# Optimization experiments

Hardware: AMD Instinct MI355X
Metric: run time of the kernel (lower is better)

Reference implementation:

```python
import jax, jax.numpy as jnp
import numpy as np

N_USER = 150_000
M_ITEM = 30_000
N_NODES = N_USER + M_ITEM
D = 64                      # embedding_dim
N_LAYERS = 3                # gcn_layer_number
E = 600_000                 # user-item interactions (symmetric nnz = 2E)
B = 1024
NUM_RATE, NUM_GENRE, NUM_DIR, NUM_ACT = 6, 25, 2186, 8030
NUM_GENDER, NUM_AGE, NUM_OCC, NUM_ZIP = 2, 7, 21, 3402
H1, H2 = 64, 64             # first/second fc hidden dims
FC1_IN = D * 10


def setup_inputs() -> dict:
    key = jax.random.key(0)
    ks = jax.random.split(key, 24)
    # aux features: 0/1 values are valid indices for every categorical field
    aux_info = jax.random.randint(ks[0], (B, 10246), 0, 2, dtype=jnp.int32)
    user_ids = jax.random.randint(ks[1], (B,), 0, N_USER, dtype=jnp.int32)
    item_ids = jax.random.randint(ks[2], (B,), 0, M_ITEM, dtype=jnp.int32)
    # bipartite graph: random interactions, symmetric normalized adjacency
    u = jax.random.randint(ks[3], (E,), 0, N_USER, dtype=jnp.int32)
    i = jax.random.randint(ks[4], (E,), 0, M_ITEM, dtype=jnp.int32) + N_USER
    graph_row = jnp.concatenate([u, i])
    graph_col = jnpph = jnp.concatenate([i, u]) if False else jnp.concatenate([i, u])
    deg = jax.ops.segment_sum(jnp.ones((2 * E,), jnp.float32), graph_row, num_segments=N_NODES)
    dinv = jnp.where(deg > 0, jax.lax.rsqrt(jnp.maximum(deg, 1.0)), 0.0)
    graph_val = dinv[graph_row] * dinv[graph_col]
    s = 0.1
    nrm = lambda k, shp: (jax.random.normal(k, shp, jnp.float32) * s)
    return {
        "aux_info": aux_info, "user_ids": user_ids, "item_ids": item_ids,
        "graph_row": graph_row, "graph_col": graph_col, "graph_val": graph_val,
        "rate_tab": nrm(ks[5], (NUM_RATE, D)),
        "genre_W": nrm(ks[6], (NUM_GENRE, D)),
        "director_W": nrm(ks[7], (NUM_DIR, D)),
        "actor_W": nrm(ks[8], (NUM_ACT, D)),
        "gender_tab": nrm(ks[9], (NUM_GENDER, D)),
        "age_tab": nrm(ks[10], (NUM_AGE, D)),
        "occ_tab": nrm(ks[11], (NUM_OCC, D)),
        "area_tab": nrm(ks[12], (NUM_ZIP, D)),
        "user_rel": nrm(ks[13], (N_USER, D)),
        "item_rel": nrm(ks[14], (M_ITEM, D)),
        "fc1_W": nrm(ks[15], (FC1_IN, H1)), "fc1_b": jnp.zeros((H1,), jnp.float32),
        "fc2_W": nrm(ks[16], (H1, H2)), "fc2_b": jnp.zeros((H2,), jnp.float32),
        "out_W": nrm(ks[17], (H2, 1)), "out_b": jnp.zeros((1,), jnp.float32),
    }


def _lightgcn(user_rel, item_rel, row, col, val):
    # LightGCN: repeated SpMM D^-1/2 A D^-1/2 @ emb, mean over layer outputs
    emb = jnp.concatenate([user_rel, item_rel], axis=0)      # [N, D]
    acc = emb
    for _ in range(N_LAYERS):
        emb = jax.ops.segment_sum(val[:, None] * emb[col], row, num_segments=N_NODES)
        acc = acc + emb
    light = acc / (N_LAYERS + 1)
    return light[:N_USER], light[N_USER:]


def _multi_hot(idx_int, W):
    x = idx_int.astype(jnp.float32)
    return (x @ W) / jnp.sum(x, axis=1, keepdims=True)


def reference(aux_info, user_ids, item_ids, graph_row, graph_col, graph_val,
              rate_tab, genre_W, director_W, actor_W,
              gender_tab, age_tab, occ_tab, area_tab,
              user_rel, item_rel,
              fc1_W, fc1_b, fc2_W, fc2_b, out_W, out_b):
    rate_idx = aux_info[:, 0]
    genre_idx = aux_info[:, 1:26]
    director_idx = aux_info[:, 26:2212]
    actor_idx = aux_info[:, 2212:10242]
    gender_idx = aux_info[:, 10242]
    age_idx = aux_info[:, 10243]
    occ_idx = aux_info[:, 10244]
    area_idx = aux_info[:, 10245]

    item_emb = jnp.concatenate([
        rate_tab[rate_idx],
        _multi_hot(genre_idx, genre_W),
        _multi_hot(director_idx, director_W),
        _multi_hot(actor_idx, actor_W),
    ], axis=1)                                               # [B, 4D]
    user_emb = jnp.concatenate([
        gender_tab[gender_idx], age_tab[age_idx],
        occ_tab[occ_idx], area_tab[area_idx],
    ], axis=1)                                               # [B, 4D]

    all_users, all_items = _lightgcn(user_rel, item_rel, graph_row, graph_col, graph_val)
    X = jnp.concatenate([item_emb, user_emb,
                         all_users[user_ids], all_items[item_ids]], axis=1)  # [B, 10D]
    X = jax.nn.relu(X @ fc1_W + fc1_b)
    X = jax.nn.relu(X @ fc2_W + fc2_b)
    return X @ out_W + out_b                                 # [B, 1]
```

## Files before the change

kernel.cpp:

```cpp
#include <hip/hip_runtime.h>
#include <hip/hip_bf16.h>
#include <hip/hip_fp16.h>

#define N_USER 150000
#define M_ITEM 30000
#define N_NODES 180000
#define E2 1200000
#define BATCH 1024
#define AUX_W 10246
#define KP_G 32
#define KP_D 2208
#define KP_A 8064
#define NBKT 265
#define WT_BLKS 2576
#define BCNT_BLKS 293
#define MH_BLKS 672

typedef __attribute__((ext_vector_type(8))) short short8;
typedef __attribute__((ext_vector_type(8))) unsigned short ushort8_t;
typedef __attribute__((ext_vector_type(4))) float f32x4;

__device__ __forceinline__ int bucket_of(int r) {
    return r < N_USER ? (r >> 10) : 147 + ((r - N_USER) >> 8);
}

__device__ __forceinline__ int detect_f32(const void* probe) {
    float v = __bfloat162float(((const __hip_bfloat16*)probe)[threadIdx.x & 63]);
    unsigned long long m = __ballot(!(fabsf(v) < 1000.0f));
    return __popcll(m) > 8;
}

struct CvtSeg { const void* src; float* dst; int n; int blk0; };
struct CvtBatch { CvtSeg seg[16]; };

__global__ void __launch_bounds__(256) k_prep(CvtBatch cb, int cvtBlks,
                                              const void* Wg, const void* Wd, const void* Wa,
                                              unsigned short* WtG, unsigned short* WtD, unsigned short* WtA,
                                              const int* __restrict__ grow, int* __restrict__ bucket_tot,
                                              const void* probe) {
    int blk = blockIdx.x, tid = threadIdx.x;
    if (blk < cvtBlks) {
        int isf32 = detect_f32(probe);
        int si = 0;
        #pragma unroll
        for (int i = 0; i < 16; ++i) if (blk >= cb.seg[i].blk0) si = i;
        const CvtSeg sg = cb.seg[si];
        int i = (blk - sg.blk0) * 256 + tid;
        if (i >= sg.n) return;
        if (isf32) sg.dst[i] = ((const float*)sg.src)[i];
        else       sg.dst[i] = __bfloat162float(((const __hip_bfloat16*)sg.src)[i]);
        return;
    }
    if (blk < cvtBlks + WT_BLKS) {
        int isf32 = detect_f32(probe);
        int t = (blk - cvtBlks) * 256 + tid;
        if (t >= (KP_G + KP_D + KP_A) * 64) return;
        int kp = t >> 6, n = t & 63;
        int k, K; const void* src; unsigned short* dst;
        if (kp < KP_G)              { k = kp;               K = 25;   src = Wg; dst = WtG; }
        else if (kp < KP_G + KP_D)  { k = kp - KP_G;        K = 2186; src = Wd; dst = WtD; }
        else                        { k = kp - KP_G - KP_D; K = 8030; src = Wa; dst = WtA; }
        unsigned short v = 0;
        if (k < K) {
            if (isf32) {
                __hip_bfloat16 h = __float2bfloat16(((const float*)src)[(size_t)k * 64 + n]);
                v = *(unsigned short*)&h;
            } else {
                v = ((const unsigned short*)src)[(size_t)k * 64 + n];
            }
        }
        dst[(((size_t)(k >> 5) * 64 + n) * 4 + ((k >> 3) & 3)) * 8 + (k & 7)] = v;
        return;
    }
    __shared__ int h[NBKT];
    for (int i = tid; i < NBKT; i += 256) h[i] = 0;
    __syncthreads();
    int idx0 = (blk - cvtBlks - WT_BLKS) * 4096;
    #pragma unroll
    for (int k = 0; k < 16; ++k) {
        int i = idx0 + k * 256 + tid;
        if (i < E2) atomicAdd(&h[bucket_of(grow[i])], 1);
    }
    __syncthreads();
    for (int i = tid; i < NBKT; i += 256) if (h[i]) atomicAdd(&bucket_tot[i], h[i]);
}

__global__ void __launch_bounds__(512) k_bscan(const int* __restrict__ bucket_tot,
                                               int* __restrict__ bucket_base,
                                               int* __restrict__ bucketcur) {
    __shared__ int s[512];
    int tid = threadIdx.x;
    s[tid] = (tid < NBKT) ? bucket_tot[tid] : 0;
    __syncthreads();
    for (int off = 1; off < 512; off <<= 1) {
        int v = (tid >= off) ? s[tid - off] : 0;
        __syncthreads();
        s[tid] += v;
        __syncthreads();
    }
    int excl = tid ? s[tid - 1] : 0;
    bucket_base[tid] = excl;
    if (tid < NBKT) bucketcur[tid] = excl;
}

__device__ void mhgemm_body(int blk, const int* __restrict__ aux,
                            const unsigned short* __restrict__ WtG,
                            const unsigned short* __restrict__ WtD,
                            const unsigned short* __restrict__ WtA,
                            float* __restrict__ Xmh, float* __restrict__ cntf) {
    int seg, rb, k0, klen, Kseg, auxoff;
    const unsigned short* Wt;
    if (blk < 16)       { seg = 0; rb = blk;                      k0 = 0;              klen = 25;                  Kseg = 25;   auxoff = 1;    Wt = WtG; }
    else if (blk < 160) { int t = blk - 16;  seg = 1; rb = t & 15; k0 = (t >> 4) * 256; klen = min(256, 2186 - k0); Kseg = 2186; auxoff = 26;   Wt = WtD; }
    else                { int t = blk - 160; seg = 2; rb = t & 15; k0 = (t >> 4) * 256; klen = min(256, 8030 - k0); Kseg = 8030; auxoff = 2212; Wt = WtA; }
    int lane = threadIdx.x & 63, wave = threadIdx.x >> 6;
    int m = lane & 15, quad = lane >> 4;
    int row = rb * 64 + wave * 16 + m;
    const int* arow = aux + (size_t)row * AUX_W + auxoff;

    f32x4 acc0 = {0.f,0.f,0.f,0.f}, acc1 = acc0, acc2 = acc0, acc3 = acc0;
    int isum = 0;
    int nchunk = (klen + 31) >> 5;
    int pa[8], na[8];
    auto lda = [&](int kci, int (&A)[8]) {
        int kb = k0 + kci * 32 + quad * 8;
        if (kb + 8 <= Kseg) {
            #pragma unroll
            for (int j = 0; j < 8; ++j) A[j] = arow[kb + j];
        } else {
            #pragma unroll
            for (int j = 0; j < 8; ++j) A[j] = (kb + j < Kseg) ? arow[kb + j] : 0;
        }
    };
    lda(0, pa);
    for (int kci = 0; kci < nchunk; ++kci) {
        if (kci + 1 < nchunk) lda(kci + 1, na);
        union { unsigned u[4]; short8 s; } af;
        af.u[0] = (unsigned)pa[0] * 16256u + (unsigned)pa[1] * 0x3F800000u;
        af.u[1] = (unsigned)pa[2] * 16256u + (unsigned)pa[3] * 0x3F800000u;
        af.u[2] = (unsigned)pa[4] * 16256u + (unsigned)pa[5] * 0x3F800000u;
        af.u[3] = (unsigned)pa[6] * 16256u + (unsigned)pa[7] * 0x3F800000u;
        isum += pa[0] + pa[1] + pa[2] + pa[3] + pa[4] + pa[5] + pa[6] + pa[7];
        size_t kcg = (size_t)(k0 >> 5) + kci;
        const unsigned short* bp = Wt + ((kcg * 64 + m) * 4 + quad) * 8;
        short8 b0 = *(const short8*)(bp);
        short8 b1 = *(const short8*)(bp + 512);
        short8 b2 = *(const short8*)(bp + 1024);
        short8 b3 = *(const short8*)(bp + 1536);
        acc0 = __builtin_amdgcn_mfma_f32_16x16x32_bf16(af.s, b0, acc0, 0, 0, 0);
        acc1 = __builtin_amdgcn_mfma_f32_16x16x32_bf16(af.s, b1, acc1, 0, 0, 0);
        acc2 = __builtin_amdgcn_mfma_f32_16x16x32_bf16(af.s, b2, acc2, 0, 0, 0);
        acc3 = __builtin_amdgcn_mfma_f32_16x16x32_bf16(af.s, b3, acc3, 0, 0, 0);
        #pragma unroll
        for (int j = 0; j < 8; ++j) pa[j] = na[j];
    }
    float asum = (float)isum;
    asum += __shfl_xor(asum, 16);
    asum += __shfl_xor(asum, 32);
    if (quad == 0) atomicAdd(&cntf[seg * BATCH + row], asum);
    float* xbase = Xmh + ((size_t)seg * BATCH + rb * 64 + wave * 16 + quad * 4) * 64;
    #pragma unroll
    for (int reg = 0; reg < 4; ++reg) {
        float* xr = xbase + (size_t)reg * 64;
        atomicAdd(&xr[ 0 + m], acc0[reg]);
        atomicAdd(&xr[16 + m], acc1[reg]);
        atomicAdd(&xr[32 + m], acc2[reg]);
        atomicAdd(&xr[48 + m], acc3[reg]);
    }
}

__global__ void __launch_bounds__(256) k_p1(const int* __restrict__ grow, const int* __restrict__ gcol,
                                            int* __restrict__ bucketcur, int2* __restrict__ binned,
                                            const int* __restrict__ aux,
                                            const unsigned short* __restrict__ WtG,
                                            const unsigned short* __restrict__ WtD,
                                            const unsigned short* __restrict__ WtA,
                                            float* __restrict__ Xmh, float* __restrict__ cntf) {
    if (blockIdx.x < MH_BLKS) {
        mhgemm_body(blockIdx.x, aux, WtG, WtD, WtA, Xmh, cntf);
        return;
    }
    __shared__ int h1[NBKT], base1[NBKT];
    int tid = threadIdx.x;
    for (int i = tid; i < NBKT; i += 256) h1[i] = 0;
    __syncthreads();
    int idx0 = (blockIdx.x - MH_BLKS) * 4096;
    int r[16], c[16];
    #pragma unroll
    for (int k = 0; k < 16; ++k) {
        int i = idx0 + k * 256 + tid;
        if (i < E2) {
            r[k] = grow[i]; c[k] = gcol[i];
            atomicAdd(&h1[bucket_of(r[k])], 1);
        } else r[k] = -1;
    }
    __syncthreads();
    for (int i = tid; i < NBKT; i += 256) {
        base1[i] = h1[i] ? atomicAdd(&bucketcur[i], h1[i]) : 0;
        h1[i] = 0;
    }
    __syncthreads();
    #pragma unroll
    for (int k = 0; k < 16; ++k) {
        if (r[k] >= 0) {
            int b = bucket_of(r[k]);
            int p = base1[b] + atomicAdd(&h1[b], 1);
            binned[p] = make_int2(r[k], c[k]);
        }
    }
}

__global__ void __launch_bounds__(256) k_p2(const int2* __restrict__ binned, const int* __restrict__ bb,
                                            int* __restrict__ cols, int2* __restrict__ moffs,
                                            float* __restrict__ dinv, float* __restrict__ dsq,
                                            float* __restrict__ gsc) {
    __shared__ int h[1024];
    __shared__ int ws2[256];
    int b = blockIdx.x, tid = threadIdx.x;
    int r0, r1;
    if (b < 147) { r0 = b << 10; r1 = min((b + 1) << 10, N_USER); }
    else         { r0 = N_USER + ((b - 147) << 8); r1 = min(N_USER + ((b - 146) << 8), N_NODES); }
    int s0 = bb[b], e0 = bb[b + 1];
    for (int i = tid; i < 1024; i += 256) h[i] = 0;
    __syncthreads();
    for (int j = s0 + tid; j < e0; j += 256) atomicAdd(&h[binned[j].x - r0], 1);
    __syncthreads();
    int t0 = tid * 4;
    int a0 = h[t0], a1 = h[t0 + 1], a2 = h[t0 + 2], a3 = h[t0 + 3];
    ws2[tid] = a0 + a1 + a2 + a3;
    __syncthreads();
    for (int off = 1; off < 256; off <<= 1) {
        int v = (tid >= off) ? ws2[tid - off] : 0;
        __syncthreads();
        ws2[tid] += v;
        __syncthreads();
    }
    int excl = tid ? ws2[tid - 1] : 0;
    int ex[4] = { excl, excl + a0, excl + a0 + a1, excl + a0 + a1 + a2 };
    int ac[4] = { a0, a1, a2, a3 };
    #pragma unroll
    for (int i = 0; i < 4; ++i) {
        int row = r0 + t0 + i;
        if (row < r1) {
            moffs[row] = make_int2(s0 + ex[i], s0 + ex[i] + ac[i]);
            float deg = (float)ac[i];
            bool nz = deg > 0.f;
            dinv[row] = nz ? rsqrtf(deg) : 0.f;
            dsq[row]  = nz ? 1.f / deg  : 0.f;
            gsc[row]  = nz ? sqrtf(deg) : 0.f;
        }
        h[t0 + i] = ex[i];
    }
    __syncthreads();
    for (int j = s0 + tid; j < e0; j += 256) {
        int2 e = binned[j];
        int p = s0 + atomicAdd(&h[e.x - r0], 1);
        cols[p] = e.y << 7;
    }
}

__global__ void __launch_bounds__(256) k_cvt_fused(const void* rawU, const void* rawI,
                                                   const float* __restrict__ dinv,
                                                   __half* __restrict__ emb,
                                                   float* __restrict__ tacc,
                                                   const int* __restrict__ uids,
                                                   const int* __restrict__ iids, int cvtN,
                                                   const int2* __restrict__ moffs,
                                                   const int* __restrict__ cols,
                                                   int2* __restrict__ moffs2) {
    int blk = blockIdx.x;
    if (blk < cvtN) {
        int isf32 = detect_f32(rawU);
        int q = blk * 256 + threadIdx.x;
        if (q >= N_NODES * 8) return;
        int r = q >> 3;
        const void* src; size_t qq;
        if (r < N_USER) { src = rawU; qq = (size_t)q; }
        else            { src = rawI; qq = (size_t)q - (size_t)N_USER * 8; }
        float d = dinv[r];
        float f[8];
        if (isf32) {
            float4 a = ((const float4*)src)[qq * 2], b = ((const float4*)src)[qq * 2 + 1];
            f[0]=a.x; f[1]=a.y; f[2]=a.z; f[3]=a.w; f[4]=b.x; f[5]=b.y; f[6]=b.z; f[7]=b.w;
        } else {
            ushort8_t u = ((const ushort8_t*)src)[qq];
            #pragma unroll
            for (int i = 0; i < 8; ++i) {
                unsigned short us = u[i];
                f[i] = __bfloat162float(*(__hip_bfloat16*)&us);
            }
        }
        ushort8_t o;
        #pragma unroll
        for (int i = 0; i < 8; ++i) {
            __half h = __float2half(f[i] * d);
            o[i] = *(unsigned short*)&h;
        }
        ((ushort8_t*)emb)[(size_t)q] = o;
        return;
    }
    if (blk < cvtN + 512) {
        int lane = threadIdx.x & 63;
        int t = (blk - cvtN) * 4 + (threadIdx.x >> 6);
        int r = (t < BATCH) ? uids[t] : (N_USER + iids[t - BATCH]);
        int2 se = moffs[r];
        if (lane == 0) moffs2[r] = se;
        for (int j = se.x + lane; j < se.y; j += 64) {
            int c = (unsigned)cols[j] >> 7;
            moffs2[c] = moffs[c];
        }
        return;
    }
    {
        int isf32 = detect_f32(rawU);
        int lane = threadIdx.x & 63;
        int t = (blk - cvtN - 512) * 4 + (threadIdx.x >> 6);
        const void* src; size_t ri;
        if (t < BATCH) { src = rawU; ri = (size_t)uids[t]; }
        else           { src = rawI; ri = (size_t)iids[t - BATCH]; }
        float v;
        if (isf32) v = ((const float*)src)[ri * 64 + lane];
        else       v = __bfloat162float(((const __hip_bfloat16*)src)[ri * 64 + lane]);
        tacc[(size_t)t * 64 + lane] = v;
    }
}

__global__ void __launch_bounds__(256, 8) k_spmv(const __half* __restrict__ src, __half* __restrict__ dst,
                                                 const int2* __restrict__ moffs_in, const int* __restrict__ cols,
                                                 const float* __restrict__ dsq,
                                                 int spmvN, float* __restrict__ tacc,
                                                 const int* __restrict__ uids, const int* __restrict__ iids,
                                                 const float* __restrict__ gsc) {
    int tid = threadIdx.x, lane = tid & 63;
    int blk = blockIdx.x;
    if (blk >= spmvN) {
        int t = (blk - spmvN) * 4 + (tid >> 6);
        int r = (t < BATCH) ? uids[t] : (N_USER + iids[t - BATCH]);
        tacc[(size_t)t * 64 + lane] += __half2float(src[(size_t)r * 64 + lane]) * gsc[r];
        return;
    }
    int wid8 = blk * 4 + (tid >> 6);
    int g = lane >> 3, l8 = lane & 7;
    int r = wid8 * 8 + g;
    int2 se = moffs_in[r];
    int s = se.x, e = se.y;
    const char* sb = (const char*)src + (l8 << 4);
    float2 a0 = {0.f,0.f}, a1 = a0, a2 = a0, a3 = a0;
    int j0 = s;
    for (; j0 + 4 <= e; j0 += 4) {
        int c[4];
        #pragma unroll
        for (int u = 0; u < 4; ++u) c[u] = cols[j0 + u];
        float4 rv[4];
        #pragma unroll
        for (int u = 0; u < 4; ++u) rv[u] = *(const float4*)(sb + (size_t)(unsigned)c[u]);
        #pragma unroll
        for (int u = 0; u < 4; ++u) {
            const __half2* h = (const __half2*)&rv[u];
            float2 f0 = __half22float2(h[0]), f1 = __half22float2(h[1]);
            float2 f2 = __half22float2(h[2]), f3 = __half22float2(h[3]);
            a0.x += f0.x; a0.y += f0.y; a1.x += f1.x; a1.y += f1.y;
            a2.x += f2.x; a2.y += f2.y; a3.x += f3.x; a3.y += f3.y;
        }
    }
    if (j0 < e) {
        int c[4]; float w[4];
        #pragma unroll
        for (int u = 0; u < 4; ++u) {
            int j = j0 + u;
            c[u] = cols[min(j, e - 1)];
            w[u] = (j < e) ? 1.f : 0.f;
        }
        float4 rv[4];
        #pragma unroll
        for (int u = 0; u < 4; ++u) rv[u] = *(const float4*)(sb + (size_t)(unsigned)c[u]);
        #pragma unroll
        for (int u = 0; u < 4; ++u) {
            const __half2* h = (const __half2*)&rv[u];
            float2 f0 = __half22float2(h[0]), f1 = __half22float2(h[1]);
            float2 f2 = __half22float2(h[2]), f3 = __half22float2(h[3]);
            a0.x = fmaf(w[u], f0.x, a0.x); a0.y = fmaf(w[u], f0.y, a0.y);
            a1.x = fmaf(w[u], f1.x, a1.x); a1.y = fmaf(w[u], f1.y, a1.y);
            a2.x = fmaf(w[u], f2.x, a2.x); a2.y = fmaf(w[u], f2.y, a2.y);
            a3.x = fmaf(w[u], f3.x, a3.x); a3.y = fmaf(w[u], f3.y, a3.y);
        }
    }
    if (e > s) {
        float d = dsq[r];
        float4 ov;
        __half2* op = (__half2*)&ov;
        op[0] = __floats2half2_rn(a0.x * d, a0.y * d);
        op[1] = __floats2half2_rn(a1.x * d, a1.y * d);
        op[2] = __floats2half2_rn(a2.x * d, a2.y * d);
        op[3] = __floats2half2_rn(a3.x * d, a3.y * d);
        *(float4*)((char*)dst + ((size_t)r << 7) + (l8 << 4)) = ov;
    }
}

__global__ void __launch_bounds__(256) k_spmv3(const __half* __restrict__ src, float* __restrict__ tacc,
                                               const int2* __restrict__ moffs, const int* __restrict__ cols,
                                               const float* __restrict__ dinv, const float* __restrict__ gsc,
                                               const int* __restrict__ uids, const int* __restrict__ iids) {
    int tid = threadIdx.x, lane = tid & 63;
    int t = blockIdx.x * 4 + (tid >> 6);
    if (t >= 2048) return;
    int r = (t < BATCH) ? uids[t] : (N_USER + iids[t - BATCH]);
    int2 se = moffs[r];
    int s = se.x, e = se.y;
    int p = lane & 31, ep = lane >> 5;
    const char* sb = (const char*)src + (p << 2);
    float ax = 0.f, ay = 0.f;
    int j0 = s;
    for (; j0 + 16 <= e; j0 += 16) {
        int c[8];
        #pragma unroll
        for (int u = 0; u < 8; ++u) c[u] = cols[j0 + 2 * u + ep];
        float2 v[8];
        #pragma unroll
        for (int u = 0; u < 8; ++u) v[u] = __half22float2(*(const __half2*)(sb + (size_t)(unsigned)c[u]));
        #pragma unroll
        for (int u = 0; u < 8; ++u) { ax += v[u].x; ay += v[u].y; }
    }
    if (j0 + 8 <= e) {
        int c[4];
        #pragma unroll
        for (int u = 0; u < 4; ++u) c[u] = cols[j0 + 2 * u + ep];
        float2 v[4];
        #pragma unroll
        for (int u = 0; u < 4; ++u) v[u] = __half22float2(*(const __half2*)(sb + (size_t)(unsigned)c[u]));
        #pragma unroll
        for (int u = 0; u < 4; ++u) { ax += v[u].x; ay += v[u].y; }
        j0 += 8;
    }
    if (j0 + 4 <= e) {
        int c0 = cols[j0 + ep], c1 = cols[j0 + 2 + ep];
        float2 v0 = __half22float2(*(const __half2*)(sb + (size_t)(unsigned)c0));
        float2 v1 = __half22float2(*(const __half2*)(sb + (size_t)(unsigned)c1));
        ax += v0.x + v1.x; ay += v0.y + v1.y;
        j0 += 4;
    }
    if (j0 < e) {
        int j1 = j0 + ep, j2 = j0 + 2 + ep;
        int c0 = cols[min(j1, e - 1)], c1 = cols[min(j2, e - 1)];
        float w0 = (j1 < e) ? 1.f : 0.f, w1 = (j2 < e) ? 1.f : 0.f;
        float2 v0 = __half22float2(*(const __half2*)(sb + (size_t)(unsigned)c0));
        float2 v1 = __half22float2(*(const __half2*)(sb + (size_t)(unsigned)c1));
        ax = fmaf(w0, v0.x, ax); ay = fmaf(w0, v0.y, ay);
        ax = fmaf(w1, v1.x, ax); ay = fmaf(w1, v1.y, ay);
    }
    ax += __shfl_xor(ax, 32);
    ay += __shfl_xor(ay, 32);
    if (ep == 0) {
        float2 self = __half22float2(*(const __half2*)((const char*)src + ((size_t)r << 7) + (p << 2)));
        float di = dinv[r], g = gsc[r];
        float* tp = tacc + (size_t)t * 64 + (p << 1);
        tp[0] += di * ax + g * self.x;
        tp[1] += di * ay + g * self.y;
    }
}

__global__ void __launch_bounds__(256) k_mlp(const int* __restrict__ aux,
                                             const float* __restrict__ ratef, const float* __restrict__ genderf,
                                             const float* __restrict__ agef, const float* __restrict__ occf,
                                             const float* __restrict__ areaf, const float* __restrict__ tacc,
                                             const float* __restrict__ Xmh, const float* __restrict__ cntf,
                                             const float* __restrict__ W1, const float* __restrict__ b1,
                                             const float* __restrict__ W2, const float* __restrict__ b2,
                                             const float* __restrict__ Wo, const float* __restrict__ bo,
                                             void* __restrict__ out, const void* probe) {
    __shared__ float sx[4][640];
    __shared__ float sh[4][64];
    int isf32 = detect_f32(probe);
    int lane = threadIdx.x & 63, w = threadIdx.x >> 6;
    int b = blockIdx.x * 4 + w;
    const int* arow = aux + (size_t)b * AUX_W;
    float* xr = sx[w];
    xr[0   + lane] = ratef[arow[0] * 64 + lane];
    xr[64  + lane] = Xmh[((size_t)0 * BATCH + b) * 64 + lane] / cntf[0 * BATCH + b];
    xr[128 + lane] = Xmh[((size_t)1 * BATCH + b) * 64 + lane] / cntf[1 * BATCH + b];
    xr[192 + lane] = Xmh[((size_t)2 * BATCH + b) * 64 + lane] / cntf[2 * BATCH + b];
    xr[256 + lane] = genderf[arow[10242] * 64 + lane];
    xr[320 + lane] = agef[arow[10243] * 64 + lane];
    xr[384 + lane] = occf[arow[10244] * 64 + lane];
    xr[448 + lane] = areaf[arow[10245] * 64 + lane];
    xr[512 + lane] = tacc[(size_t)b * 64 + lane] * 0.25f;
    xr[576 + lane] = tacc[(size_t)(BATCH + b) * 64 + lane] * 0.25f;
    float acc = b1[lane];
    #pragma unroll 8
    for (int k = 0; k < 640; ++k) acc += xr[k] * W1[(size_t)k * 64 + lane];
    float h1 = fmaxf(acc, 0.f);
    sh[w][lane] = h1;
    float acc2 = b2[lane];
    #pragma unroll 8
    for (int j = 0; j < 64; ++j) acc2 += sh[w][j] * W2[(size_t)j * 64 + lane];
    float h2 = fmaxf(acc2, 0.f);
    float p = h2 * Wo[lane];
    #pragma unroll
    for (int off = 32; off; off >>= 1) p += __shfl_down(p, off);
    if (lane == 0) {
        float r = p + bo[0];
        if (isf32) ((float*)out)[b] = r;
        else       ((__hip_bfloat16*)out)[b] = __float2bfloat16(r);
    }
}

extern "C" void kernel_launch(void* const* d_in, const int* in_sizes, int n_in,
                              void* d_out, int out_size, void* d_ws, size_t ws_size,
                              hipStream_t stream) {
    const int* aux  = (const int*)d_in[0];
    const int* uids = (const int*)d_in[1];
    const int* iids = (const int*)d_in[2];
    const int* grow = (const int*)d_in[3];
    const int* gcol = (const int*)d_in[4];

    char* p = (char*)d_ws;
    auto alloc = [&](size_t bytes) -> char* {
        char* r = p;
        p += (bytes + 255) / 256 * 256;
        return r;
    };
    int*   bucket_tot  = (int*)alloc(512 * 4);
    float* Xmh         = (float*)alloc((size_t)3 * BATCH * 64 * 4);
    float* cntf        = (float*)alloc((size_t)3 * BATCH * 4);
    int2*  moffs2      = (int2*)alloc((size_t)180224 * 8);
    char*  zero_end    = p;
    int*   bucket_base = (int*)alloc(512 * 4);
    int*   bucketcur   = (int*)alloc(512 * 4);
    int2*  moffs       = (int2*)alloc((size_t)180224 * 8);
    float* dinv        = (float*)alloc((size_t)180224 * 4);
    float* dsq         = (float*)alloc((size_t)180224 * 4);
    float* gsc         = (float*)alloc((size_t)180224 * 4);
    int2*  binned      = (int2*)alloc((size_t)E2 * 8);
    int*   cols        = (int*)alloc((size_t)E2 * 4);
    __half* embA       = (__half*)alloc((size_t)N_NODES * 64 * 2);
    __half* embB       = (__half*)alloc((size_t)N_NODES * 64 * 2);
    float* tacc        = (float*)alloc((size_t)2048 * 64 * 4);
    unsigned short* WtG = (unsigned short*)alloc((size_t)KP_G * 64 * 2);
    unsigned short* WtD = (unsigned short*)alloc((size_t)KP_D * 64 * 2);
    unsigned short* WtA = (unsigned short*)alloc((size_t)KP_A * 64 * 2);
    float* ratef   = (float*)alloc(384 * 4);
    float* genderf = (float*)alloc(128 * 4);
    float* agef    = (float*)alloc(448 * 4);
    float* occf    = (float*)alloc(1344 * 4);
    float* areaf   = (float*)alloc((size_t)217728 * 4);
    float* fc1W    = (float*)alloc((size_t)40960 * 4);
    float* fc1b    = (float*)alloc(64 * 4);
    float* fc2W    = (float*)alloc(4096 * 4);
    float* fc2b    = (float*)alloc(64 * 4);
    float* outW    = (float*)alloc(64 * 4);
    float* outb    = (float*)alloc(4);

    const void* probe = d_in[14];

    hipMemsetAsync(bucket_tot, 0, (size_t)(zero_end - (char*)bucket_tot), stream);

    CvtBatch cb;
    int blk = 0, si = 0;
    auto addseg = [&](const void* s, float* d, int n) {
        cb.seg[si].src = s; cb.seg[si].dst = d; cb.seg[si].n = n; cb.seg[si].blk0 = blk;
        blk += (n + 255) / 256; ++si;
    };
    addseg(d_in[6],  ratef,   384);
    addseg(d_in[10], genderf, 128);
    addseg(d_in[11], agef,    448);
    addseg(d_in[12], occf,    1344);
    addseg(d_in[13], areaf,   217728);
    addseg(d_in[16], fc1W,   40960);
    addseg(d_in[17], fc1b,   64);
    addseg(d_in[18], fc2W,   4096);
    addseg(d_in[19], fc2b,   64);
    addseg(d_in[20], outW,   64);
    addseg(d_in[21], outb,   1);
    for (int i = si; i < 16; ++i) { cb.seg[i].src = nullptr; cb.seg[i].dst = nullptr; cb.seg[i].n = 0; cb.seg[i].blk0 = 0x7fffffff; }
    const int cvtBlks = blk;
    hipLaunchKernelGGL(k_prep, dim3(cvtBlks + WT_BLKS + BCNT_BLKS), dim3(256), 0, stream,
                       cb, cvtBlks, d_in[7], d_in[8], d_in[9], WtG, WtD, WtA, grow, bucket_tot, probe);

    hipLaunchKernelGGL(k_bscan, dim3(1), dim3(512), 0, stream, bucket_tot, bucket_base, bucketcur);
    hipLaunchKernelGGL(k_p1, dim3(MH_BLKS + (E2 + 4095) / 4096), dim3(256), 0, stream,
                       grow, gcol, bucketcur, binned, aux, WtG, WtD, WtA, Xmh, cntf);
    hipLaunchKernelGGL(k_p2, dim3(NBKT), dim3(256), 0, stream, binned, bucket_base, cols, moffs, dinv, dsq, gsc);

    const int cvtN = (N_NODES * 8 + 255) / 256;
    hipLaunchKernelGGL(k_cvt_fused, dim3(cvtN + 1024), dim3(256), 0, stream,
                       d_in[14], d_in[15], dinv, embA, tacc, uids, iids, cvtN,
                       moffs, cols, moffs2);

    const int spmvN = N_NODES / 32;
    hipLaunchKernelGGL(k_spmv, dim3(spmvN), dim3(256), 0, stream,
                       embA, embB, moffs, cols, dsq, spmvN, (float*)nullptr, uids, iids, gsc);
    hipLaunchKernelGGL(k_spmv, dim3(spmvN + 512), dim3(256), 0, stream,
                       embB, embA, moffs2, cols, dsq, spmvN, tacc, uids, iids, gsc);
    hipLaunchKernelGGL(k_spmv3, dim3(2048 / 4), dim3(256), 0, stream,
                       embA, tacc, moffs, cols, dinv, gsc, uids, iids);

    hipLaunchKernelGGL(k_mlp, dim3(BATCH / 4), dim3(256), 0, stream,
                       aux, ratef, genderf, agef, occf, areaf, tacc, Xmh, cntf,
                       fc1W, fc1b, fc2W, fc2b, outW, outb, d_out, probe);
}
```

Measured before the change: 295.0 us.

## Compute degrees early and fold embedding conversion into earlier kernels

```diff
diff --git a/kernel.cpp b/kernel.cpp
--- a/kernel.cpp
+++ b/kernel.cpp
@@ -15,6 +15,7 @@
 #define WT_BLKS 2576
 #define BCNT_BLKS 293
 #define MH_BLKS 672
+#define CVT_BLKS 5625
 
 typedef __attribute__((ext_vector_type(8))) short short8;
 typedef __attribute__((ext_vector_type(8))) unsigned short ushort8_t;
@@ -37,7 +38,7 @@
                                               const void* Wg, const void* Wd, const void* Wa,
                                               unsigned short* WtG, unsigned short* WtD, unsigned short* WtA,
                                               const int* __restrict__ grow, int* __restrict__ bucket_tot,
-                                              const void* probe) {
+                                              int* __restrict__ deg, const void* probe) {
     int blk = blockIdx.x, tid = threadIdx.x;
     if (blk < cvtBlks) {
         int isf32 = detect_f32(probe);
@@ -79,7 +80,11 @@
     #pragma unroll
     for (int k = 0; k < 16; ++k) {
         int i = idx0 + k * 256 + tid;
-        if (i < E2) atomicAdd(&h[bucket_of(grow[i])], 1);
+        if (i < E2) {
+            int r = grow[i];
+            atomicAdd(&h[bucket_of(r)], 1);
+            atomicAdd(&deg[r], 1);
+        }
     }
     __syncthreads();
     for (int i = tid; i < NBKT; i += 256) if (h[i]) atomicAdd(&bucket_tot[i], h[i]);
@@ -87,9 +92,21 @@
 
 __global__ void __launch_bounds__(512) k_bscan(const int* __restrict__ bucket_tot,
                                                int* __restrict__ bucket_base,
-                                               int* __restrict__ bucketcur) {
+                                               int* __restrict__ bucketcur,
+                                               const int* __restrict__ deg,
+                                               float* __restrict__ dinv, float* __restrict__ dsq,
+                                               float* __restrict__ gsc) {
+    int tid = threadIdx.x;
+    if (blockIdx.x > 0) {
+        int r = (blockIdx.x - 1) * 512 + tid;
+        float d = (float)deg[r];
+        bool nz = d > 0.f;
+        dinv[r] = nz ? rsqrtf(d) : 0.f;
+        dsq[r]  = nz ? 1.f / d  : 0.f;
+        gsc[r]  = nz ? sqrtf(d) : 0.f;
+        return;
+    }
     __shared__ int s[512];
-    int tid = threadIdx.x;
     s[tid] = (tid < NBKT) ? bucket_tot[tid] : 0;
     __syncthreads();
     for (int off = 1; off < 512; off <<= 1) {
@@ -175,45 +192,77 @@
                                             const unsigned short* __restrict__ WtG,
                                             const unsigned short* __restrict__ WtD,
                                             const unsigned short* __restrict__ WtA,
-                                            float* __restrict__ Xmh, float* __restrict__ cntf) {
-    if (blockIdx.x < MH_BLKS) {
-        mhgemm_body(blockIdx.x, aux, WtG, WtD, WtA, Xmh, cntf);
+                                            float* __restrict__ Xmh, float* __restrict__ cntf,
+                                            const void* rawU, const void* rawI,
+                                            const float* __restrict__ dinv,
+                                            __half* __restrict__ emb) {
+    int blk = blockIdx.x;
+    if (blk < MH_BLKS) {
+        mhgemm_body(blk, aux, WtG, WtD, WtA, Xmh, cntf);
         return;
     }
-    __shared__ int h1[NBKT], base1[NBKT];
-    int tid = threadIdx.x;
-    for (int i = tid; i < NBKT; i += 256) h1[i] = 0;
-    __syncthreads();
-    int idx0 = (blockIdx.x - MH_BLKS) * 4096;
-    int r[16], c[16];
+    if (blk < MH_BLKS + BCNT_BLKS) {
+        __shared__ int h1[NBKT], base1[NBKT];
+        int tid = threadIdx.x;
+        for (int i = tid; i < NBKT; i += 256) h1[i] = 0;
+        __syncthreads();
+        int idx0 = (blk - MH_BLKS) * 4096;
+        int r[16], c[16];
+        #pragma unroll
+        for (int k = 0; k < 16; ++k) {
+            int i = idx0 + k * 256 + tid;
+            if (i < E2) {
+                r[k] = grow[i]; c[k] = gcol[i];
+                atomicAdd(&h1[bucket_of(r[k])], 1);
+            } else r[k] = -1;
+        }
+        __syncthreads();
+        for (int i = tid; i < NBKT; i += 256) {
+            base1[i] = h1[i] ? atomicAdd(&bucketcur[i], h1[i]) : 0;
+            h1[i] = 0;
+        }
+        __syncthreads();
+        #pragma unroll
+        for (int k = 0; k < 16; ++k) {
+            if (r[k] >= 0) {
+                int b = bucket_of(r[k]);
+                int p = base1[b] + atomicAdd(&h1[b], 1);
+                binned[p] = make_int2(r[k], c[k]);
+            }
+        }
+        return;
+    }
+    int isf32 = detect_f32(rawU);
+    int q = (blk - MH_BLKS - BCNT_BLKS) * 256 + threadIdx.x;
+    if (q >= N_NODES * 8) return;
+    int r = q >> 3;
+    const void* src; size_t qq;
+    if (r < N_USER) { src = rawU; qq = (size_t)q; }
+    else            { src = rawI; qq = (size_t)q - (size_t)N_USER * 8; }
+    float d = dinv[r];
+    float f[8];
+    if (isf32) {
+        float4 a = ((const float4*)src)[qq * 2], b = ((const float4*)src)[qq * 2 + 1];
+        f[0]=a.x; f[1]=a.y; f[2]=a.z; f[3]=a.w; f[4]=b.x; f[5]=b.y; f[6]=b.z; f[7]=b.w;
+    } else {
+        ushort8_t u = ((const ushort8_t*)src)[qq];
+        #pragma unroll
+        for (int i = 0; i < 8; ++i) {
+            unsigned short us = u[i];
+            f[i] = __bfloat162float(*(__hip_bfloat16*)&us);
+        }
+    }
+    ushort8_t o;
     #pragma unroll
-    for (int k = 0; k < 16; ++k) {
-        int i = idx0 + k * 256 + tid;
-        if (i < E2) {
-            r[k] = grow[i]; c[k] = gcol[i];
-            atomicAdd(&h1[bucket_of(r[k])], 1);
-        } else r[k] = -1;
-    }
-    __syncthreads();
-    for (int i = tid; i < NBKT; i += 256) {
-        base1[i] = h1[i] ? atomicAdd(&bucketcur[i], h1[i]) : 0;
-        h1[i] = 0;
-    }
-    __syncthreads();
-    #pragma unroll
-    for (int k = 0; k < 16; ++k) {
-        if (r[k] >= 0) {
-            int b = bucket_of(r[k]);
-            int p = base1[b] + atomicAdd(&h1[b], 1);
-            binned[p] = make_int2(r[k], c[k]);
-        }
-    }
+    for (int i = 0; i < 8; ++i) {
+        __half h = __float2half(f[i] * d);
+        o[i] = *(unsigned short*)&h;
+    }
+    ((ushort8_t*)emb)[(size_t)q] = o;
 }
 
 __global__ void __launch_bounds__(256) k_p2(const int2* __restrict__ binned, const int* __restrict__ bb,
-                                            int* __restrict__ cols, int2* __restrict__ moffs,
-                                            float* __restrict__ dinv, float* __restrict__ dsq,
-                                            float* __restrict__ gsc) {
+                                            int* __restrict__ cols, int2* __restrict__ moffs) {
     __shared__ int h[1024];
     __shared__ int ws2[256];
     int b = blockIdx.x, tid = threadIdx.x;
@@ -241,14 +290,7 @@
     #pragma unroll
     for (int i = 0; i < 4; ++i) {
         int row = r0 + t0 + i;
-        if (row < r1) {
-            moffs[row] = make_int2(s0 + ex[i], s0 + ex[i] + ac[i]);
-            float deg = (float)ac[i];
-            bool nz = deg > 0.f;
-            dinv[row] = nz ? rsqrtf(deg) : 0.f;
-            dsq[row]  = nz ? 1.f / deg  : 0.f;
-            gsc[row]  = nz ? sqrtf(deg) : 0.f;
-        }
+        if (row < r1) moffs[row] = make_int2(s0 + ex[i], s0 + ex[i] + ac[i]);
         h[t0 + i] = ex[i];
     }
     __syncthreads();
@@ -259,85 +301,46 @@
     }
 }
 
-__global__ void __launch_bounds__(256) k_cvt_fused(const void* rawU, const void* rawI,
-                                                   const float* __restrict__ dinv,
-                                                   __half* __restrict__ emb,
-                                                   float* __restrict__ tacc,
-                                                   const int* __restrict__ uids,
-                                                   const int* __restrict__ iids, int cvtN,
-                                                   const int2* __restrict__ moffs,
-                                                   const int* __restrict__ cols,
-                                                   int2* __restrict__ moffs2) {
-    int blk = blockIdx.x;
-    if (blk < cvtN) {
-        int isf32 = detect_f32(rawU);
-        int q = blk * 256 + threadIdx.x;
-        if (q >= N_NODES * 8) return;
-        int r = q >> 3;
-        const void* src; size_t qq;
-        if (r < N_USER) { src = rawU; qq = (size_t)q; }
-        else            { src = rawI; qq = (size_t)q - (size_t)N_USER * 8; }
-        float d = dinv[r];
-        float f[8];
-        if (isf32) {
-            float4 a = ((const float4*)src)[qq * 2], b = ((const float4*)src)[qq * 2 + 1];
-            f[0]=a.x; f[1]=a.y; f[2]=a.z; f[3]=a.w; f[4]=b.x; f[5]=b.y; f[6]=b.z; f[7]=b.w;
-        } else {
-            ushort8_t u = ((const ushort8_t*)src)[qq];
-            #pragma unroll
-            for (int i = 0; i < 8; ++i) {
-                unsigned short us = u[i];
-                f[i] = __bfloat162float(*(__hip_bfloat16*)&us);
-            }
-        }
-        ushort8_t o;
-        #pragma unroll
-        for (int i = 0; i < 8; ++i) {
-            __half h = __float2half(f[i] * d);
-            o[i] = *(unsigned short*)&h;
-        }
-        ((ushort8_t*)emb)[(size_t)q] = o;
-        return;
-    }
-    if (blk < cvtN + 512) {
-        int lane = threadIdx.x & 63;
-        int t = (blk - cvtN) * 4 + (threadIdx.x >> 6);
-        int r = (t < BATCH) ? uids[t] : (N_USER + iids[t - BATCH]);
-        int2 se = moffs[r];
-        if (lane == 0) moffs2[r] = se;
-        for (int j = se.x + lane; j < se.y; j += 64) {
-            int c = (unsigned)cols[j] >> 7;
-            moffs2[c] = moffs[c];
-        }
-        return;
-    }
-    {
-        int isf32 = detect_f32(rawU);
-        int lane = threadIdx.x & 63;
-        int t = (blk - cvtN - 512) * 4 + (threadIdx.x >> 6);
-        const void* src; size_t ri;
-        if (t < BATCH) { src = rawU; ri = (size_t)uids[t]; }
-        else           { src = rawI; ri = (size_t)iids[t - BATCH]; }
-        float v;
-        if (isf32) v = ((const float*)src)[ri * 64 + lane];
-        else       v = __bfloat162float(((const __hip_bfloat16*)src)[ri * 64 + lane]);
-        tacc[(size_t)t * 64 + lane] = v;
-    }
-}
-
 __global__ void __launch_bounds__(256, 8) k_spmv(const __half* __restrict__ src, __half* __restrict__ dst,
                                                  const int2* __restrict__ moffs_in, const int* __restrict__ cols,
                                                  const float* __restrict__ dsq,
                                                  int spmvN, float* __restrict__ tacc,
                                                  const int* __restrict__ uids, const int* __restrict__ iids,
-                                                 const float* __restrict__ gsc) {
+                                                 const float* __restrict__ gsc,
+                                                 const void* rawU, const void* rawI,
+                                                 int2* __restrict__ moffs2, int xmode) {
     int tid = threadIdx.x, lane = tid & 63;
     int blk = blockIdx.x;
     if (blk >= spmvN) {
-        int t = (blk - spmvN) * 4 + (tid >> 6);
-        int r = (t < BATCH) ? uids[t] : (N_USER + iids[t - BATCH]);
-        tacc[(size_t)t * 64 + lane] += __half2float(src[(size_t)r * 64 + lane]) * gsc[r];
-        return;
+        if (xmode == 1) {
+            int t = (blk - spmvN) * 4 + (tid >> 6);
+            int r = (t < BATCH) ? uids[t] : (N_USER + iids[t - BATCH]);
+            tacc[(size_t)t * 64 + lane] += __half2float(src[(size_t)r * 64 + lane]) * gsc[r];
+            return;
+        }
+        if (blk < spmvN + 512) {
+            int t = (blk - spmvN) * 4 + (tid >> 6);
+            int r = (t < BATCH) ? uids[t] : (N_USER + iids[t - BATCH]);
+            int2 se = moffs_in[r];
+            if (lane == 0) moffs2[r] = se;
+            for (int j = se.x + lane; j < se.y; j += 64) {
+                int c = (unsigned)cols[j] >> 7;
+                moffs2[c] = moffs_in[c];
+            }
+            return;
+        }
+        {
+            int isf32 = detect_f32(rawU);
+            int t = (blk - spmvN - 512) * 4 + (tid >> 6);
+            const void* s; size_t ri;
+            if (t < BATCH) { s = rawU; ri = (size_t)uids[t]; }
+            else           { s = rawI; ri = (size_t)iids[t - BATCH]; }
+            float v;
+            if (isf32) v = ((const float*)s)[ri * 64 + lane];
+            else       v = __bfloat162float(((const __hip_bfloat16*)s)[ri * 64 + lane]);
+            tacc[(size_t)t * 64 + lane] = v;
+            return;
+        }
     }
     int wid8 = blk * 4 + (tid >> 6);
     int g = lane >> 3, l8 = lane & 7;
@@ -523,6 +526,7 @@
     float* Xmh         = (float*)alloc((size_t)3 * BATCH * 64 * 4);
     float* cntf        = (float*)alloc((size_t)3 * BATCH * 4);
     int2*  moffs2      = (int2*)alloc((size_t)180224 * 8);
+    int*   deg         = (int*)alloc((size_t)180224 * 4);
     char*  zero_end    = p;
     int*   bucket_base = (int*)alloc(512 * 4);
     int*   bucketcur   = (int*)alloc(512 * 4);
@@ -574,23 +578,24 @@
     for (int i = si; i < 16; ++i) { cb.seg[i].src = nullptr; cb.seg[i].dst = nullptr; cb.seg[i].n = 0; cb.seg[i].blk0 = 0x7fffffff; }
     const int cvtBlks = blk;
     hipLaunchKernelGGL(k_prep, dim3(cvtBlks + WT_BLKS + BCNT_BLKS), dim3(256), 0, stream,
-                       cb, cvtBlks, d_in[7], d_in[8], d_in[9], WtG, WtD, WtA, grow, bucket_tot, probe);
-
-    hipLaunchKernelGGL(k_bscan, dim3(1), dim3(512), 0, stream, bucket_tot, bucket_base, bucketcur);
-    hipLaunchKernelGGL(k_p1, dim3(MH_BLKS + (E2 + 4095) / 4096), dim3(256), 0, stream,
-                       grow, gcol, bucketcur, binned, aux, WtG, WtD, WtA, Xmh, cntf);
-    hipLaunchKernelGGL(k_p2, dim3(NBKT), dim3(256), 0, stream, binned, bucket_base, cols, moffs, dinv, dsq, gsc);
-
-    const int cvtN = (N_NODES * 8 + 255) / 256;
-    hipLaunchKernelGGL(k_cvt_fused, dim3(cvtN + 1024), dim3(256), 0, stream,
-                       d_in[14], d_in[15], dinv, embA, tacc, uids, iids, cvtN,
-                       moffs, cols, moffs2);
+                       cb, cvtBlks, d_in[7], d_in[8], d_in[9], WtG, WtD, WtA, grow, bucket_tot, deg, probe);
+
+    hipLaunchKernelGGL(k_bscan, dim3(353), dim3(512), 0, stream,
+                       bucket_tot, bucket_base, bucketcur, deg, dinv, dsq, gsc);
+
+    hipLaunchKernelGGL(k_p1, dim3(MH_BLKS + BCNT_BLKS + CVT_BLKS), dim3(256), 0, stream,
+                       grow, gcol, bucketcur, binned, aux, WtG, WtD, WtA, Xmh, cntf,
+                       d_in[14], d_in[15], dinv, embA);
+
+    hipLaunchKernelGGL(k_p2, dim3(NBKT), dim3(256), 0, stream, binned, bucket_base, cols, moffs);
 
     const int spmvN = N_NODES / 32;
-    hipLaunchKernelGGL(k_spmv, dim3(spmvN), dim3(256), 0, stream,
-                       embA, embB, moffs, cols, dsq, spmvN, (float*)nullptr, uids, iids, gsc);
+    hipLaunchKernelGGL(k_spmv, dim3(spmvN + 1024), dim3(256), 0, stream,
+                       embA, embB, moffs, cols, dsq, spmvN, tacc, uids, iids, gsc,
+                       d_in[14], d_in[15], moffs2, 0);
     hipLaunchKernelGGL(k_spmv, dim3(spmvN + 512), dim3(256), 0, stream,
-                       embB, embA, moffs2, cols, dsq, spmvN, tacc, uids, iids, gsc);
+                       embB, embA, moffs2, cols, dsq, spmvN, tacc, uids, iids, gsc,
+                       d_in[14], d_in[15], moffs2, 1);
     hipLaunchKernelGGL(k_spmv3, dim3(2048 / 4), dim3(256), 0, stream,
                        embA, tacc, moffs, cols, dinv, gsc, uids, iids);
 
```

Result: slower. 327.2 us (+10.9%).
